# Kernel tuning notes

Hardware: AMD Instinct MI355X
Metric: run time of the kernel (lower is better)

The kernel has to match this reference:

```python
import jax, jax.numpy as jnp
import numpy as np

N_NODES = 50000
N_EDGES = 800000
NUM_GRAPHS = 250
NODES_PER_GRAPH = 200  # max_len for to_dense_batch
IN_DIM = 128
H1 = 128
H2 = 128
LSTM_H = 128
OUT_DIM = 2
NEG_SLOPE = 0.2  # PyG GATConv default leaky relu slope


def setup_inputs() -> dict:
    key = jax.random.key(0)
    ks = jax.random.split(key, 16)
    x = jax.random.normal(ks[0], (N_NODES, IN_DIM), dtype=jnp.float32)
    edge_index = jax.random.randint(ks[1], (2, N_EDGES), 0, N_NODES, dtype=jnp.int32)
    batch = (jnp.arange(N_NODES, dtype=jnp.int32) // NODES_PER_GRAPH)
    g = lambda k, shp, fan: jax.random.normal(k, shp, dtype=jnp.float32) / np.sqrt(fan)
    return {
        "x": x,
        "edge_index": edge_index,
        "batch": batch,
        "W_gat": g(ks[2], (IN_DIM, H1), IN_DIM),
        "a_src": g(ks[3], (H1,), H1),
        "a_dst": g(ks[4], (H1,), H1),
        "b_gat": jnp.zeros((H1,), jnp.float32),
        "W_gcn": g(ks[5], (H1, H2), H1),
        "b_gcn": jnp.zeros((H2,), jnp.float32),
        "W_ih": g(ks[6], (4 * LSTM_H, H2), H2),
        "W_hh": g(ks[7], (4 * LSTM_H, LSTM_H), LSTM_H),
        "b_ih": jnp.zeros((4 * LSTM_H,), jnp.float32),
        "b_hh": jnp.zeros((4 * LSTM_H,), jnp.float32),
        "W_fc": g(ks[8], (LSTM_H, OUT_DIM), LSTM_H),
        "b_fc": jnp.zeros((OUT_DIM,), jnp.float32),
    }


def _add_self_loops(edge_index, n):
    loop = jnp.arange(n, dtype=edge_index.dtype)
    src = jnp.concatenate([edge_index[0], loop])
    dst = jnp.concatenate([edge_index[1], loop])
    return src, dst


def _gat_conv(x, edge_index, W, a_src, a_dst, b):
    n = x.shape[0]
    h = x @ W                                  # [N, H1]
    src, dst = _add_self_loops(edge_index, n)
    alpha_s = h @ a_src                        # [N]
    alpha_d = h @ a_dst
    e = alpha_s[src] + alpha_d[dst]            # [E+N]
    e = jnp.where(e > 0, e, NEG_SLOPE * e)     # leaky relu
    # softmax over edges sharing the same destination node
    m = jax.ops.segment_max(e, dst, num_segments=n)
    ex = jnp.exp(e - m[dst])
    denom = jax.ops.segment_sum(ex, dst, num_segments=n)
    alpha = ex / denom[dst]
    out = jax.ops.segment_sum(h[src] * alpha[:, None], dst, num_segments=n)
    return out + b


def _gcn_conv(x, edge_index, W, b):
    n = x.shape[0]
    h = x @ W                                  # [N, H2]
    src, dst = _add_self_loops(edge_index, n)
    deg = jax.ops.segment_sum(jnp.ones_like(dst, dtype=h.dtype), dst, num_segments=n)
    dinv = jax.lax.rsqrt(jnp.maximum(deg, 1.0))
    coef = dinv[src] * dinv[dst]               # symmetric normalization
    out = jax.ops.segment_sum(h[src] * coef[:, None], dst, num_segments=n)
    return out + b


def _to_dense_batch(x, batch, num_graphs, max_len):
    n = x.shape[0]
    ones = jnp.ones((n,), jnp.int32)
    counts = jax.ops.segment_sum(ones, batch, num_segments=num_graphs)
    starts = jnp.cumsum(counts) - counts
    pos = jnp.arange(n, dtype=jnp.int32) - starts[batch]
    padded = jnp.zeros((num_graphs, max_len, x.shape[1]), x.dtype)
    padded = padded.at[batch, pos].set(x)
    return padded, counts


def _lstm_last_hidden(padded, lengths, W_ih, W_hh, b_ih, b_hh):
    B, T, D = padded.shape
    H = W_hh.shape[1]
    xs = jnp.swapaxes(padded, 0, 1)            # [T, B, D]

    def step(carry, x_t):
        h, c = carry
        gates = x_t @ W_ih.T + b_ih + h @ W_hh.T + b_hh
        i, f, g, o = jnp.split(gates, 4, axis=-1)
        c = jax.nn.sigmoid(f) * c + jax.nn.sigmoid(i) * jnp.tanh(g)
        h = jax.nn.sigmoid(o) * jnp.tanh(c)
        return (h, c), h

    init = (jnp.zeros((B, H), padded.dtype), jnp.zeros((B, H), padded.dtype))
    _, hs = jax.lax.scan(step, init, xs)       # hs: [T, B, H]
    # packed-sequence semantics: hidden state at each graph's last valid step
    return hs[lengths - 1, jnp.arange(B)]


def reference(x, edge_index, batch, W_gat, a_src, a_dst, b_gat, W_gcn, b_gcn,
              W_ih, W_hh, b_ih, b_hh, W_fc, b_fc):
    h = jax.nn.relu(_gat_conv(x, edge_index, W_gat, a_src, a_dst, b_gat))
    h = jax.nn.relu(_gcn_conv(h, edge_index, W_gcn, b_gcn))
    padded, lengths = _to_dense_batch(h, batch, NUM_GRAPHS, NODES_PER_GRAPH)
    g_rep = _lstm_last_hidden(padded, lengths, W_ih, W_hh, b_ih, b_hh)
    return g_rep @ W_fc + b_fc
```

## Files before the change

### kernel.cpp

```cpp
#include <hip/hip_runtime.h>
#include <cstddef>

#define NN 50000
#define NE 800000
#define NG 250
#define TT 200
#define DD 128
#define GH 512
#define NEG_SLOPE 0.2f
#define NCHUNK 4
#define CLEN 50
#define CAP 128
#define PSTRIDE 136

static __device__ __forceinline__ float fsig(float x) { return 1.0f / (1.0f + __expf(-x)); }
static __device__ __forceinline__ float ftanh(float x) {
    float e = __expf(2.0f * x);
    return 1.0f - 2.0f / (e + 1.0f);
}
static __device__ __forceinline__ unsigned short f2bf(float f) {
    unsigned int u = __float_as_uint(f);
    return (unsigned short)((u + 0x7fffu + ((u >> 16) & 1u)) >> 16);
}

static __device__ __forceinline__ void gll16(const float* src, float* ldsdst) {
    __builtin_amdgcn_global_load_lds(
        (const __attribute__((address_space(1))) void*)src,
        (__attribute__((address_space(3))) void*)ldsdst, 16, 0, 0);
}

__global__ void k_init(int* cnt, int* gstart, int n, int ng1) {
    int i = blockIdx.x * 256 + threadIdx.x;
    if (i < n) cnt[i] = 1;
    if (i < ng1) gstart[i] = n;
}

__global__ void k_transpose2(const float* __restrict__ inA, float* __restrict__ outA,
                             const float* __restrict__ inB, float* __restrict__ outB) {
    int b = blockIdx.x, k = threadIdx.x;
    if (b < DD) outA[b * DD + k] = inA[k * DD + b];
    else { int n = b - DD; outB[n * DD + k] = inB[k * DD + n]; }
}

__global__ __launch_bounds__(256) void k_gemm(
    const float* __restrict__ A, const float* __restrict__ B, float* __restrict__ C,
    int M, int N, int t0, int clen, int rowsPerGraph,
    const float* __restrict__ bias1, const float* __restrict__ bias2,
    unsigned short* __restrict__ Cbf,
    float* __restrict__ as_out, float* __restrict__ ad_out,
    const float* __restrict__ a_src, const float* __restrict__ a_dst)
{
    __shared__ float4 As[2][1024];
    __shared__ float4 Bs[2][1024];
    const int tid = threadIdx.x;
    const int wv = tid >> 6;
    const int m0 = blockIdx.x * 128, n0 = blockIdx.y * 128;
    const int tr = tid >> 4, tc = tid & 15;

    float acc[8][8];
    #pragma unroll
    for (int i = 0; i < 8; ++i)
        #pragma unroll
        for (int j = 0; j < 8; ++j) acc[i][j] = 0.f;

    auto stageA = [&](int buf, int k0) {
        #pragma unroll
        for (int it = 0; it < 4; ++it) {
            int f4 = it * 256 + tid;
            int r = f4 >> 3;
            int c4s = (f4 & 7) ^ (r & 7);
            int gr = m0 + r;
            float* dst = (float*)&As[buf][it * 256 + wv * 64];
            if (gr < M) {
                int flat = (gr / clen) * rowsPerGraph + t0 + (gr % clen);
                gll16(A + (size_t)flat * DD + k0 + c4s * 4, dst);
            }
        }
    };
    auto stageB = [&](int buf, int k0) {
        #pragma unroll
        for (int it = 0; it < 4; ++it) {
            int f4 = it * 256 + tid;
            int r = f4 >> 3;
            int c4s = (f4 & 7) ^ (r & 7);
            int gn = n0 + r;
            float* dst = (float*)&Bs[buf][it * 256 + wv * 64];
            if (gn < N) gll16(B + (size_t)gn * DD + k0 + c4s * 4, dst);
        }
    };

    stageA(0, 0); stageB(0, 0);
    __syncthreads();
    int buf = 0;
    const int axor = tr & 7;
    const int bxor = tc & 7;
    for (int ks = 0; ks < 4; ++ks) {
        if (ks < 3) { stageA(buf ^ 1, (ks + 1) * 32); stageB(buf ^ 1, (ks + 1) * 32); }
        const float4* Af = &As[buf][0];
        const float4* Bf = &Bs[buf][0];
        #pragma unroll 1
        for (int k4 = 0; k4 < 8; ++k4) {
            float4 a[8], b[8];
            #pragma unroll
            for (int i = 0; i < 8; ++i) a[i] = Af[(tr + i * 16) * 8 + (k4 ^ axor)];
            #pragma unroll
            for (int j = 0; j < 8; ++j) b[j] = Bf[(tc + j * 16) * 8 + (k4 ^ bxor)];
            #pragma unroll
            for (int i = 0; i < 8; ++i)
                #pragma unroll
                for (int j = 0; j < 8; ++j)
                    acc[i][j] += a[i].x * b[j].x + a[i].y * b[j].y + a[i].z * b[j].z + a[i].w * b[j].w;
        }
        __syncthreads();
        buf ^= 1;
    }

    if (as_out) {
        float asv[8], adv[8];
        #pragma unroll
        for (int j = 0; j < 8; ++j) { asv[j] = a_src[tc + 16 * j]; adv[j] = a_dst[tc + 16 * j]; }
        #pragma unroll
        for (int i = 0; i < 8; ++i) {
            float s = 0.f, d = 0.f;
            #pragma unroll
            for (int j = 0; j < 8; ++j) { s += acc[i][j] * asv[j]; d += acc[i][j] * adv[j]; }
            #pragma unroll
            for (int off = 1; off < 16; off <<= 1) { s += __shfl_xor(s, off); d += __shfl_xor(d, off); }
            int gr = m0 + tr + i * 16;
            if (tc == 0 && gr < M) { as_out[gr] = s; ad_out[gr] = d; }
        }
    }

    #pragma unroll
    for (int i = 0; i < 8; ++i) {
        int gr = m0 + tr + i * 16;
        if (gr >= M) continue;
        #pragma unroll
        for (int j = 0; j < 8; ++j) {
            int gn = n0 + tc + j * 16;
            if (gn >= N) continue;
            float v = acc[i][j];
            if (bias1) v += bias1[gn];
            if (bias2) v += bias2[gn];
            if (Cbf) Cbf[(size_t)gr * N + gn] = f2bf(v);
            else     C[(size_t)gr * N + gn] = v;
        }
    }
}

__global__ void k_hist(const int* __restrict__ ei, int* cnt, int E) {
    int e = blockIdx.x * 256 + threadIdx.x;
    if (e < E) atomicAdd(&cnt[ei[E + e]], 1);
}

__global__ __launch_bounds__(256) void k_scan1(const int* __restrict__ cnt, int* __restrict__ fill,
                                               int* __restrict__ bsum, int n) {
    __shared__ int wsum[4];
    int tid = threadIdx.x, lane = tid & 63, wv = tid >> 6;
    int i = blockIdx.x * 256 + tid;
    int v = (i < n) ? cnt[i] : 0;
    int sc = v;
    #pragma unroll
    for (int off = 1; off < 64; off <<= 1) {
        int t = __shfl_up(sc, off);
        if (lane >= off) sc += t;
    }
    if (lane == 63) wsum[wv] = sc;
    __syncthreads();
    int base = 0;
    if (wv > 0) base += wsum[0];
    if (wv > 1) base += wsum[1];
    if (wv > 2) base += wsum[2];
    if (i < n) fill[i] = base + sc - v;
    if (tid == 255) bsum[blockIdx.x] = base + sc;
}
__global__ __launch_bounds__(256) void k_scan2(int* __restrict__ bsum, int nb) {
    __shared__ int wsum[4];
    int tid = threadIdx.x, lane = tid & 63, wv = tid >> 6;
    int v = (tid < nb) ? bsum[tid] : 0;
    int sc = v;
    #pragma unroll
    for (int off = 1; off < 64; off <<= 1) {
        int t = __shfl_up(sc, off);
        if (lane >= off) sc += t;
    }
    if (lane == 63) wsum[wv] = sc;
    __syncthreads();
    int base = 0;
    if (wv > 0) base += wsum[0];
    if (wv > 1) base += wsum[1];
    if (wv > 2) base += wsum[2];
    if (tid < nb) bsum[tid] = base + sc - v;
}
__global__ void k_scan3(const int* __restrict__ bsum, const int* __restrict__ cnt,
                        int* __restrict__ rp, int* __restrict__ fill,
                        float* __restrict__ dinv, const int* __restrict__ batch,
                        int* __restrict__ gstart, int n) {
    int i = blockIdx.x * 256 + threadIdx.x;
    if (i >= n) return;
    int v = fill[i] + bsum[blockIdx.x];
    rp[i] = v;
    fill[i] = v;
    if (i == n - 1) rp[n] = v + cnt[i];
    dinv[i] = rsqrtf(fmaxf((float)cnt[i], 1.0f));
    int b = batch[i];
    if (i == 0 || batch[i - 1] != b) gstart[b] = i;
}

__global__ void k_fill(const int* __restrict__ ei, int* fill, int* esrc, int E, int N) {
    int i = blockIdx.x * 256 + threadIdx.x;
    if (i < E) {
        int s = ei[i], d = ei[E + i];
        int slot = atomicAdd(&fill[d], 1);
        esrc[slot] = s;
    } else if (i < E + N) {
        int v = i - E;
        int slot = atomicAdd(&fill[v], 1);
        esrc[slot] = v;
    }
}

__global__ __launch_bounds__(256) void k_gat(
    const unsigned int* __restrict__ h1b,
    const float* __restrict__ as, const float* __restrict__ ad_,
    const int* __restrict__ rp, const int* __restrict__ esrc,
    const float* __restrict__ bias, float* __restrict__ out, int n)
{
    __shared__ float2 ws_sh[4][CAP];
    int wv = threadIdx.x >> 6;
    int node = blockIdx.x * 4 + wv;
    int lane = threadIdx.x & 63;
    if (node >= n) return;
    int r0 = rp[node], r1 = rp[node + 1];
    int deg = r1 - r0;
    float adv = ad_[node];

    float sum = 0.f;
    for (int base = 0; base < deg; base += 64) {
        int idx = base + lane;
        float ex = 0.f;
        if (idx < deg) {
            int s = esrc[r0 + idx];
            float e = as[s] + adv;
            e = e > 0.f ? e : NEG_SLOPE * e;
            ex = __expf(e);
            if (idx < CAP) ws_sh[wv][idx] = make_float2(ex, __int_as_float(s));
        }
        sum += ex;
    }
    #pragma unroll
    for (int off = 1; off < 64; off <<= 1) sum += __shfl_xor(sum, off);
    float inv = 1.0f / sum;

    int nser = deg < CAP ? deg : CAP;
    int npad = (nser + 7) & ~7;
    for (int p = nser + lane; p < npad; p += 64)
        ws_sh[wv][p] = make_float2(0.f, __int_as_float(0));

    float ax = 0.f, ay = 0.f;
    float wa[8]; unsigned int va[8];
    #pragma unroll
    for (int u = 0; u < 8; ++u) {
        float2 t = ws_sh[wv][u];
        wa[u] = t.x; va[u] = h1b[(size_t)__float_as_int(t.y) * 64 + lane];
    }
    #pragma unroll 1
    for (int idx = 8; idx < npad; idx += 8) {
        float wb[8]; unsigned int vb[8];
        #pragma unroll
        for (int u = 0; u < 8; ++u) {
            float2 t = ws_sh[wv][idx + u];
            wb[u] = t.x; vb[u] = h1b[(size_t)__float_as_int(t.y) * 64 + lane];
        }
        #pragma unroll
        for (int u = 0; u < 8; ++u) {
            ax += wa[u] * __uint_as_float(va[u] << 16);
            ay += wa[u] * __uint_as_float(va[u] & 0xffff0000u);
        }
        #pragma unroll
        for (int u = 0; u < 8; ++u) { wa[u] = wb[u]; va[u] = vb[u]; }
    }
    #pragma unroll
    for (int u = 0; u < 8; ++u) {
        ax += wa[u] * __uint_as_float(va[u] << 16);
        ay += wa[u] * __uint_as_float(va[u] & 0xffff0000u);
    }

    for (int j = r0 + CAP; j < r1; ++j) {
        int s = esrc[j];
        float e = as[s] + adv;
        e = e > 0.f ? e : NEG_SLOPE * e;
        float w = __expf(e);
        unsigned int v = h1b[(size_t)s * 64 + lane];
        ax += w * __uint_as_float(v << 16);
        ay += w * __uint_as_float(v & 0xffff0000u);
    }
    float2 bv = *(const float2*)(bias + 2 * lane);
    float2 o;
    o.x = fmaxf(ax * inv + bv.x, 0.f);
    o.y = fmaxf(ay * inv + bv.y, 0.f);
    *(float2*)(out + (size_t)node * DD + 2 * lane) = o;
}

__global__ __launch_bounds__(256) void k_gcn(
    const unsigned int* __restrict__ h2b, const float* __restrict__ dinv,
    const int* __restrict__ rp, const int* __restrict__ esrc,
    const float* __restrict__ bias, const int* __restrict__ batch,
    const int* __restrict__ gstart, float* __restrict__ padded, int n)
{
    __shared__ float2 cs_sh[4][CAP];
    int wv = threadIdx.x >> 6;
    int node = blockIdx.x * 4 + wv;
    int lane = threadIdx.x & 63;
    if (node >= n) return;
    int r0 = rp[node], r1 = rp[node + 1];
    int deg = r1 - r0;
    float dn = dinv[node];

    for (int base = 0; base < deg; base += 64) {
        int idx = base + lane;
        if (idx < deg && idx < CAP) {
            int s = esrc[r0 + idx];
            cs_sh[wv][idx] = make_float2(dinv[s], __int_as_float(s));
        }
    }
    int nser = deg < CAP ? deg : CAP;
    int npad = (nser + 7) & ~7;
    for (int p = nser + lane; p < npad; p += 64)
        cs_sh[wv][p] = make_float2(0.f, __int_as_float(0));
    __syncthreads();

    float ax = 0.f, ay = 0.f;
    float wa[8]; unsigned int va[8];
    #pragma unroll
    for (int u = 0; u < 8; ++u) {
        float2 t = cs_sh[wv][u];
        wa[u] = t.x; va[u] = h2b[(size_t)__float_as_int(t.y) * 64 + lane];
    }
    #pragma unroll 1
    for (int idx = 8; idx < npad; idx += 8) {
        float wb[8]; unsigned int vb[8];
        #pragma unroll
        for (int u = 0; u < 8; ++u) {
            float2 t = cs_sh[wv][idx + u];
            wb[u] = t.x; vb[u] = h2b[(size_t)__float_as_int(t.y) * 64 + lane];
        }
        #pragma unroll
        for (int u = 0; u < 8; ++u) {
            ax += wa[u] * __uint_as_float(va[u] << 16);
            ay += wa[u] * __uint_as_float(va[u] & 0xffff0000u);
        }
        #pragma unroll
        for (int u = 0; u < 8; ++u) { wa[u] = wb[u]; va[u] = vb[u]; }
    }
    #pragma unroll
    for (int u = 0; u < 8; ++u) {
        ax += wa[u] * __uint_as_float(va[u] << 16);
        ay += wa[u] * __uint_as_float(va[u] & 0xffff0000u);
    }

    for (int j = r0 + CAP; j < r1; ++j) {
        int s = esrc[j];
        float c = dinv[s];
        unsigned int v = h2b[(size_t)s * 64 + lane];
        ax += c * __uint_as_float(v << 16);
        ay += c * __uint_as_float(v & 0xffff0000u);
    }
    int g = batch[node];
    if (g < 0 || g >= NG) return;
    int p = node - gstart[g];
    if (p < 0 || p >= TT) return;
    float2 bv = *(const float2*)(bias + 2 * lane);
    float2 o;
    o.x = fmaxf(ax * dn + bv.x, 0.f);
    o.y = fmaxf(ay * dn + bv.y, 0.f);
    *(float2*)(padded + ((size_t)g * TT + p) * DD + 2 * lane) = o;
}

__global__ __launch_bounds__(512) void k_lstm(
    const float* __restrict__ xw,
    const float* __restrict__ Whh,
    const int* __restrict__ gstart,
    float* __restrict__ hstate, float* __restrict__ cstate,
    float* __restrict__ grep, int t0, int clen)
{
    int g = blockIdx.x, tid = threadIdx.x;
    __shared__ __align__(16) float h_sh[DD];
    __shared__ __align__(16) float part[4][4 * PSTRIDE];

    const int seg = tid >> 7;
    const int gq  = tid & 127;
    const int qt  = gq >> 5;
    const int ub  = (gq & 31) * 4;
    const int u   = tid >> 2;
    const int q   = tid & 3;
    const int lane = tid & 63;
    const int qbase = lane & ~3;

    float4 w[4][8];
    #pragma unroll
    for (int g4 = 0; g4 < 4; ++g4)
        #pragma unroll
        for (int i = 0; i < 8; ++i)
            w[g4][i] = *(const float4*)(Whh + (size_t)(4 * gq + g4) * DD + seg * 32 + i * 4);

    float creg = 0.f, hn = 0.f;
    if (t0 == 0) {
        if (tid < DD) h_sh[tid] = 0.f;
    } else {
        creg = cstate[g * DD + u];
        hn = hstate[g * DD + u];
        if (q == 0) h_sh[u] = hn;
    }
    int take = gstart[g + 1] - gstart[g] - 1;
    if (take < 0) take = 0;
    if (take > TT - 1) take = TT - 1;
    __syncthreads();

    const float* xb = xw + (size_t)g * clen * GH + q * DD + u;
    float xv = xb[0];

    for (int t = t0; t < t0 + clen; ++t) {
        int rel = t - t0;
        float xvn = 0.f;
        if (rel + 1 < clen) xvn = xb[(size_t)(rel + 1) * GH];

        float4 hseg[8];
        #pragma unroll
        for (int i = 0; i < 8; ++i) hseg[i] = *(const float4*)(h_sh + seg * 32 + i * 4);
        float p0 = 0.f, p1 = 0.f, p2 = 0.f, p3 = 0.f;
        #pragma unroll
        for (int i = 0; i < 8; ++i) {
            float4 h4 = hseg[i];
            p0 += h4.x * w[0][i].x + h4.y * w[0][i].y + h4.z * w[0][i].z + h4.w * w[0][i].w;
            p1 += h4.x * w[1][i].x + h4.y * w[1][i].y + h4.z * w[1][i].z + h4.w * w[1][i].w;
            p2 += h4.x * w[2][i].x + h4.y * w[2][i].y + h4.z * w[2][i].z + h4.w * w[2][i].w;
            p3 += h4.x * w[3][i].x + h4.y * w[3][i].y + h4.z * w[3][i].z + h4.w * w[3][i].w;
        }
        *(float4*)(&part[seg][qt * PSTRIDE + ub]) = make_float4(p0, p1, p2, p3);
        __syncthreads();

        int pidx = q * PSTRIDE + u;
        float G = xv + part[0][pidx] + part[1][pidx] + part[2][pidx] + part[3][pidx];
        float a = (q == 2) ? 2.f : -1.f;
        float e = __expf(a * G);
        float act = (q == 2) ? (1.f - 2.f / (e + 1.f)) : (1.f / (1.f + e));
        float ai = __shfl(act, qbase + 0);
        float af = __shfl(act, qbase + 1);
        float ag = __shfl(act, qbase + 2);
        float ao = __shfl(act, qbase + 3);
        creg = af * creg + ai * ag;
        hn = ao * ftanh(creg);
        if (q == 0) {
            h_sh[u] = hn;
            if (t == take) grep[g * DD + u] = hn;
        }
        xv = xvn;
        __syncthreads();
    }
    if (q == 0) { hstate[g * DD + u] = hn; cstate[g * DD + u] = creg; }
}

__global__ void k_fc(const float* __restrict__ grep, const float* __restrict__ Wfc,
                     const float* __restrict__ bfc, float* __restrict__ out, int G) {
    int i = blockIdx.x * 256 + threadIdx.x;
    if (i >= G * 2) return;
    int g = i >> 1, o = i & 1;
    float acc = bfc[o];
    for (int d = 0; d < DD; ++d) acc += grep[g * DD + d] * Wfc[d * 2 + o];
    out[i] = acc;
}

extern "C" void kernel_launch(void* const* d_in, const int* in_sizes, int n_in,
                              void* d_out, int out_size, void* d_ws, size_t ws_size,
                              hipStream_t stream) {
    const float* x     = (const float*)d_in[0];
    const int*   ei    = (const int*)d_in[1];
    const int*   batch = (const int*)d_in[2];
    const float* Wgat  = (const float*)d_in[3];
    const float* a_src = (const float*)d_in[4];
    const float* a_dst = (const float*)d_in[5];
    const float* b_gat = (const float*)d_in[6];
    const float* Wgcn  = (const float*)d_in[7];
    const float* b_gcn = (const float*)d_in[8];
    const float* Wih   = (const float*)d_in[9];
    const float* Whh   = (const float*)d_in[10];
    const float* b_ih  = (const float*)d_in[11];
    const float* b_hh  = (const float*)d_in[12];
    const float* Wfc   = (const float*)d_in[13];
    const float* b_fc  = (const float*)d_in[14];
    float* out = (float*)d_out;

    float* ws = (float*)d_ws;
    const size_t F = (size_t)NN * DD;
    unsigned short* h1b = (unsigned short*)ws;
    unsigned short* h2b = (unsigned short*)ws;
    float* xwChunk = ws;
    float* gato   = ws + F;
    float* padded = ws + F;
    size_t off = 2 * F;
    float* alpha_s = ws + off; off += 50048;
    float* alpha_d = ws + off; off += 50048;
    float* dinv    = ws + off; off += 50048;
    int*   cnt     = (int*)(ws + off); off += 50048;
    int*   rp      = (int*)(ws + off); off += 50056;
    int*   fill    = (int*)(ws + off); off += 50048;
    int*   esrc    = (int*)(ws + off); off += 850048;
    int*   bsum    = (int*)(ws + off); off += 256;
    int*   gstart  = (int*)(ws + off); off += 256;
    float* grep    = ws + off; off += 32000;
    float* hstate  = ws + off; off += 32000;
    float* cstate  = ws + off; off += 32000;
    float* WgatT   = ws + off; off += 16384;
    float* WgcnT   = ws + off; off += 16384;
    const size_t xwBigFloats = (size_t)NG * TT * GH;
    float* xwBig = ws + off;
    const bool big = ws_size >= (off + xwBigFloats) * sizeof(float);

    k_transpose2<<<256, 128, 0, stream>>>(Wgat, WgatT, Wgcn, WgcnT);

    k_gemm<<<dim3(391, 1), 256, 0, stream>>>(x, WgatT, nullptr, NN, DD, 0, TT, TT,
                                             nullptr, nullptr, h1b,
                                             alpha_s, alpha_d, a_src, a_dst);

    k_init<<<196, 256, 0, stream>>>(cnt, gstart, NN, NG + 1);
    k_hist<<<3125, 256, 0, stream>>>(ei, cnt, NE);
    k_scan1<<<196, 256, 0, stream>>>(cnt, fill, bsum, NN);
    k_scan2<<<1, 256, 0, stream>>>(bsum, 196);
    k_scan3<<<196, 256, 0, stream>>>(bsum, cnt, rp, fill, dinv, batch, gstart, NN);
    k_fill<<<3321, 256, 0, stream>>>(ei, fill, esrc, NE, NN);

    k_gat<<<12500, 256, 0, stream>>>((const unsigned int*)h1b, alpha_s, alpha_d,
                                     rp, esrc, b_gat, gato, NN);

    k_gemm<<<dim3(391, 1), 256, 0, stream>>>(gato, WgcnT, nullptr, NN, DD, 0, TT, TT,
                                             nullptr, nullptr, h2b,
                                             nullptr, nullptr, nullptr, nullptr);

    k_gcn<<<12500, 256, 0, stream>>>((const unsigned int*)h2b, dinv, rp, esrc,
                                     b_gcn, batch, gstart, padded, NN);

    if (big) {
        k_gemm<<<dim3(391, 4), 256, 0, stream>>>(padded, Wih, xwBig, NG * TT, GH,
                                                 0, TT, TT, b_ih, b_hh,
                                                 nullptr, nullptr, nullptr, nullptr, nullptr);
        k_lstm<<<NG, 512, 0, stream>>>(xwBig, Whh, gstart, hstate, cstate, grep, 0, TT);
    } else {
        for (int c = 0; c < NCHUNK; ++c) {
            int t0 = c * CLEN;
            k_gemm<<<dim3(98, 4), 256, 0, stream>>>(padded, Wih, xwChunk, NG * CLEN, GH,
                                                    t0, CLEN, TT, b_ih, b_hh,
                                                    nullptr, nullptr, nullptr, nullptr, nullptr);
            k_lstm<<<NG, 512, 0, stream>>>(xwChunk, Whh, gstart, hstate, cstate, grep, t0, CLEN);
        }
    }

    k_fc<<<2, 256, 0, stream>>>(grep, Wfc, b_fc, out, NG);
}
```

Measured before the change: 577.2 us.

## Batch 16 graphs per block in LSTM recurrence using split-bf16 MFMA

Adds a new LSTM kernel that processes 16 graphs per block and computes the recurrent h@W_hh product with bf16 MFMA instructions. It keeps fp32-like accuracy by splitting weights and hidden state into hi/lo bf16 parts and issuing three MFMAs per tile. W_hh stays in registers, the hidden state is double-buffered in swizzled LDS, and the next step's input projection is prefetched. The goal is to cut the serial per-step cost of the recurrence, which was done with scalar FMAs, one graph per block. In exchange only 16 blocks are launched, so the GPU is heavily underused, and the split-bf16 scheme carries a small precision risk.

```diff
diff --git a/kernel.cpp b/kernel.cpp
--- a/kernel.cpp
+++ b/kernel.cpp
@@ -12,6 +12,10 @@
 #define CLEN 50
 #define CAP 128
 #define PSTRIDE 136
+#define GB 16
+
+typedef __attribute__((ext_vector_type(8))) short bf16x8;
+typedef __attribute__((ext_vector_type(4))) float f32x4;
 
 static __device__ __forceinline__ float fsig(float x) { return 1.0f / (1.0f + __expf(-x)); }
 static __device__ __forceinline__ float ftanh(float x) {
@@ -21,6 +25,9 @@
 static __device__ __forceinline__ unsigned short f2bf(float f) {
     unsigned int u = __float_as_uint(f);
     return (unsigned short)((u + 0x7fffu + ((u >> 16) & 1u)) >> 16);
+}
+static __device__ __forceinline__ float bf2f(unsigned short b) {
+    return __uint_as_float(((unsigned int)b) << 16);
 }
 
 static __device__ __forceinline__ void gll16(const float* src, float* ldsdst) {
@@ -377,9 +384,121 @@
     *(float2*)(padded + ((size_t)g * TT + p) * DD + 2 * lane) = o;
 }
 
-__global__ __launch_bounds__(512) void k_lstm(
+__global__ __launch_bounds__(512, 1) void k_lstm_mfma(
     const float* __restrict__ xw,
     const float* __restrict__ Whh,
+    const int* __restrict__ gstart,
+    float* __restrict__ grep)
+{
+    const int tid = threadIdx.x;
+    const int w = tid >> 6;
+    const int l = tid & 63;
+    const int col = l & 15;
+    const int kg = l >> 4;
+    const int g = blockIdx.x * GB + col;
+    const int gc = g < NG ? g : NG - 1;
+    const int urow = kg * 4;
+
+    __shared__ unsigned short hh[2][16 * 128];
+    __shared__ unsigned short hl[2][16 * 128];
+
+    bf16x8 whi[4][4], wlo[4][4];
+    #pragma unroll
+    for (int q = 0; q < 4; ++q) {
+        const float* wrow = Whh + (size_t)(q * DD + 16 * w + col) * DD;
+        #pragma unroll
+        for (int ks = 0; ks < 4; ++ks) {
+            float4 f0 = *(const float4*)(wrow + ks * 32 + kg * 8);
+            float4 f1 = *(const float4*)(wrow + ks * 32 + kg * 8 + 4);
+            float ff[8] = {f0.x, f0.y, f0.z, f0.w, f1.x, f1.y, f1.z, f1.w};
+            #pragma unroll
+            for (int j = 0; j < 8; ++j) {
+                unsigned short hi = f2bf(ff[j]);
+                whi[q][ks][j] = (short)hi;
+                wlo[q][ks][j] = (short)f2bf(ff[j] - bf2f(hi));
+            }
+        }
+    }
+
+    for (int i = tid; i < 16 * 128; i += 512) { hh[0][i] = 0; hl[0][i] = 0; }
+
+    int take = gstart[gc + 1] - gstart[gc] - 1;
+    if (take < 0) take = 0;
+    if (take > TT - 1) take = TT - 1;
+
+    float c0 = 0.f, c1 = 0.f, c2 = 0.f, c3 = 0.f;
+
+    const float* xbase = xw + (size_t)gc * TT * GH + 16 * w + urow;
+    float4 xq[4];
+    #pragma unroll
+    for (int q = 0; q < 4; ++q) xq[q] = *(const float4*)(xbase + q * DD);
+
+    const int swz = (col & 7) << 4;
+    __syncthreads();
+
+    int cur = 0;
+    for (int t = 0; t < TT; ++t) {
+        float4 xn[4];
+        if (t + 1 < TT) {
+            const float* xr = xbase + (size_t)(t + 1) * GH;
+            #pragma unroll
+            for (int q = 0; q < 4; ++q) xn[q] = *(const float4*)(xr + q * DD);
+        }
+        bf16x8 bhi[4], blo[4];
+        #pragma unroll
+        for (int ks = 0; ks < 4; ++ks) {
+            int idx = col * 128 + (((ks * 64 + kg * 16) ^ swz) >> 1);
+            bhi[ks] = *(const bf16x8*)(&hh[cur][idx]);
+            blo[ks] = *(const bf16x8*)(&hl[cur][idx]);
+        }
+        f32x4 acc[4];
+        #pragma unroll
+        for (int q = 0; q < 4; ++q) {
+            acc[q][0] = xq[q].x; acc[q][1] = xq[q].y; acc[q][2] = xq[q].z; acc[q][3] = xq[q].w;
+        }
+        #pragma unroll
+        for (int q = 0; q < 4; ++q)
+            #pragma unroll
+            for (int ks = 0; ks < 4; ++ks) {
+                acc[q] = __builtin_amdgcn_mfma_f32_16x16x32_bf16(whi[q][ks], bhi[ks], acc[q], 0, 0, 0);
+                acc[q] = __builtin_amdgcn_mfma_f32_16x16x32_bf16(whi[q][ks], blo[ks], acc[q], 0, 0, 0);
+                acc[q] = __builtin_amdgcn_mfma_f32_16x16x32_bf16(wlo[q][ks], bhi[ks], acc[q], 0, 0, 0);
+            }
+        float hv[4];
+        {
+            float ci[4] = {c0, c1, c2, c3};
+            #pragma unroll
+            for (int r = 0; r < 4; ++r) {
+                float cc = fsig(acc[1][r]) * ci[r] + fsig(acc[0][r]) * ftanh(acc[2][r]);
+                hv[r] = fsig(acc[3][r]) * ftanh(cc);
+                ci[r] = cc;
+            }
+            c0 = ci[0]; c1 = ci[1]; c2 = ci[2]; c3 = ci[3];
+        }
+        {
+            int idx = col * 128 + (((2 * (16 * w + urow)) ^ swz) >> 1);
+            unsigned short vh[4], vl[4];
+            #pragma unroll
+            for (int r = 0; r < 4; ++r) {
+                vh[r] = f2bf(hv[r]);
+                vl[r] = f2bf(hv[r] - bf2f(vh[r]));
+            }
+            *(ushort4*)(&hh[cur ^ 1][idx]) = make_ushort4(vh[0], vh[1], vh[2], vh[3]);
+            *(ushort4*)(&hl[cur ^ 1][idx]) = make_ushort4(vl[0], vl[1], vl[2], vl[3]);
+        }
+        if (t == take && g < NG) {
+            *(float4*)(grep + (size_t)g * DD + 16 * w + urow) =
+                make_float4(hv[0], hv[1], hv[2], hv[3]);
+        }
+        #pragma unroll
+        for (int q = 0; q < 4; ++q) xq[q] = xn[q];
+        cur ^= 1;
+        __syncthreads();
+    }
+}
+
+__global__ __launch_bounds__(512) void k_lstm(
+    const float* __restrict__ xw, const float* __restrict__ Whh,
     const int* __restrict__ gstart,
     float* __restrict__ hstate, float* __restrict__ cstate,
     float* __restrict__ grep, int t0, int clen)
@@ -544,7 +663,7 @@
         k_gemm<<<dim3(391, 4), 256, 0, stream>>>(padded, Wih, xwBig, NG * TT, GH,
                                                  0, TT, TT, b_ih, b_hh,
                                                  nullptr, nullptr, nullptr, nullptr, nullptr);
-        k_lstm<<<NG, 512, 0, stream>>>(xwBig, Whh, gstart, hstate, cstate, grep, 0, TT);
+        k_lstm_mfma<<<(NG + GB - 1) / GB, 512, 0, stream>>>(xwBig, Whh, gstart, grep);
     } else {
         for (int c = 0; c < NCHUNK; ++c) {
             int t0 = c * CLEN;
```

Result: slower. 825.3 us (+43.0%).

## Use split-bf16 MFMA GEMM for LSTM input projection

Applied to the files above, without the earlier changes.

Replaces the FP32 scalar GEMM computing the LSTM input projection (padded @ W_ih^T + biases) with a matrix-core kernel using bf16 MFMA 16x16x32. Near-FP32 accuracy is kept by a three-term split (A_hi*B_hi + A_lo*B_hi + A_hi*B_lo), with the A tile staged in swizzled LDS through global_load_lds. This targets the cost of a 50000x512x128 FP32 GEMM on vector ALUs, at the price of three MFMA passes plus per-element bf16 conversion work. It only applies on the 'big' path; the chunked path still uses the old GEMM.

```diff
diff --git a/kernel.cpp b/kernel.cpp
--- a/kernel.cpp
+++ b/kernel.cpp
@@ -13,6 +13,9 @@
 #define CAP 128
 #define PSTRIDE 136
 
+typedef __attribute__((ext_vector_type(8))) short bf16x8;
+typedef __attribute__((ext_vector_type(4))) float f32x4;
+
 static __device__ __forceinline__ float fsig(float x) { return 1.0f / (1.0f + __expf(-x)); }
 static __device__ __forceinline__ float ftanh(float x) {
     float e = __expf(2.0f * x);
@@ -21,6 +24,9 @@
 static __device__ __forceinline__ unsigned short f2bf(float f) {
     unsigned int u = __float_as_uint(f);
     return (unsigned short)((u + 0x7fffu + ((u >> 16) & 1u)) >> 16);
+}
+static __device__ __forceinline__ float bf2f(unsigned short b) {
+    return __uint_as_float(((unsigned int)b) << 16);
 }
 
 static __device__ __forceinline__ void gll16(const float* src, float* ldsdst) {
@@ -148,6 +154,124 @@
     }
 }
 
+__global__ __launch_bounds__(256) void k_gemm_mx(
+    const float* __restrict__ A, const float* __restrict__ Bw, float* __restrict__ C,
+    int M, int N, const float* __restrict__ bias1, const float* __restrict__ bias2)
+{
+    __shared__ float4 As[4096];
+    const int tid = threadIdx.x;
+    const int wv = tid >> 6;
+    const int l = tid & 63;
+    const int m0 = blockIdx.x * 128, n0 = blockIdx.y * 128;
+    const int wr = (wv >> 1) * 64, wc = (wv & 1) * 64;
+    const int lr = l & 15, kg = l >> 4;
+
+    #pragma unroll
+    for (int it = 0; it < 16; ++it) {
+        int f4 = it * 256 + tid;
+        int r = f4 >> 5, c4 = f4 & 31;
+        int c4s = c4 ^ (r & 7);
+        int gr = m0 + r;
+        float* dst = (float*)&As[it * 256 + wv * 64];
+        if (gr < M) gll16(A + (size_t)gr * DD + c4s * 4, dst);
+    }
+
+    bf16x8 bh[4][4];
+    #pragma unroll
+    for (int ct = 0; ct < 4; ++ct) {
+        const float* brow = Bw + (size_t)(n0 + wc + ct * 16 + lr) * DD;
+        #pragma unroll
+        for (int ks = 0; ks < 4; ++ks) {
+            float4 f0 = *(const float4*)(brow + ks * 32 + kg * 8);
+            float4 f1 = *(const float4*)(brow + ks * 32 + kg * 8 + 4);
+            float ff[8] = {f0.x, f0.y, f0.z, f0.w, f1.x, f1.y, f1.z, f1.w};
+            #pragma unroll
+            for (int j = 0; j < 8; ++j) bh[ct][ks][j] = (short)f2bf(ff[j]);
+        }
+    }
+    __syncthreads();
+
+    f32x4 acc[4][4];
+    #pragma unroll
+    for (int rt = 0; rt < 4; ++rt)
+        #pragma unroll
+        for (int ct = 0; ct < 4; ++ct) acc[rt][ct] = (f32x4){0.f, 0.f, 0.f, 0.f};
+
+    #pragma unroll 1
+    for (int ks = 0; ks < 4; ++ks) {
+        bf16x8 ahi[4], alo[4];
+        #pragma unroll
+        for (int rt = 0; rt < 4; ++rt) {
+            int row = wr + rt * 16 + lr;
+            int qb = ks * 8 + kg * 2;
+            float4 f0 = As[row * 32 + (qb ^ (row & 7))];
+            float4 f1 = As[row * 32 + ((qb + 1) ^ (row & 7))];
+            float ff[8] = {f0.x, f0.y, f0.z, f0.w, f1.x, f1.y, f1.z, f1.w};
+            #pragma unroll
+            for (int j = 0; j < 8; ++j) {
+                unsigned short hi = f2bf(ff[j]);
+                ahi[rt][j] = (short)hi;
+                alo[rt][j] = (short)f2bf(ff[j] - bf2f(hi));
+            }
+        }
+        #pragma unroll
+        for (int rt = 0; rt < 4; ++rt)
+            #pragma unroll
+            for (int ct = 0; ct < 4; ++ct) {
+                acc[rt][ct] = __builtin_amdgcn_mfma_f32_16x16x32_bf16(ahi[rt], bh[ct][ks], acc[rt][ct], 0, 0, 0);
+                acc[rt][ct] = __builtin_amdgcn_mfma_f32_16x16x32_bf16(alo[rt], bh[ct][ks], acc[rt][ct], 0, 0, 0);
+            }
+    }
+
+    #pragma unroll
+    for (int ct = 0; ct < 4; ++ct) {
+        const float* brow = Bw + (size_t)(n0 + wc + ct * 16 + lr) * DD;
+        #pragma unroll
+        for (int ks = 0; ks < 4; ++ks) {
+            float4 f0 = *(const float4*)(brow + ks * 32 + kg * 8);
+            float4 f1 = *(const float4*)(brow + ks * 32 + kg * 8 + 4);
+            float ff[8] = {f0.x, f0.y, f0.z, f0.w, f1.x, f1.y, f1.z, f1.w};
+            #pragma unroll
+            for (int j = 0; j < 8; ++j)
+                bh[ct][ks][j] = (short)f2bf(ff[j] - bf2f(f2bf(ff[j])));
+        }
+    }
+
+    #pragma unroll 1
+    for (int ks = 0; ks < 4; ++ks) {
+        bf16x8 ahi[4];
+        #pragma unroll
+        for (int rt = 0; rt < 4; ++rt) {
+            int row = wr + rt * 16 + lr;
+            int qb = ks * 8 + kg * 2;
+            float4 f0 = As[row * 32 + (qb ^ (row & 7))];
+            float4 f1 = As[row * 32 + ((qb + 1) ^ (row & 7))];
+            float ff[8] = {f0.x, f0.y, f0.z, f0.w, f1.x, f1.y, f1.z, f1.w};
+            #pragma unroll
+            for (int j = 0; j < 8; ++j) ahi[rt][j] = (short)f2bf(ff[j]);
+        }
+        #pragma unroll
+        for (int rt = 0; rt < 4; ++rt)
+            #pragma unroll
+            for (int ct = 0; ct < 4; ++ct)
+                acc[rt][ct] = __builtin_amdgcn_mfma_f32_16x16x32_bf16(ahi[rt], bh[ct][ks], acc[rt][ct], 0, 0, 0);
+    }
+
+    #pragma unroll
+    for (int ct = 0; ct < 4; ++ct) {
+        int col = n0 + wc + ct * 16 + lr;
+        float bsum = bias1[col] + bias2[col];
+        #pragma unroll
+        for (int rt = 0; rt < 4; ++rt) {
+            #pragma unroll
+            for (int r = 0; r < 4; ++r) {
+                int row = m0 + wr + rt * 16 + kg * 4 + r;
+                if (row < M) C[(size_t)row * N + col] = acc[rt][ct][r] + bsum;
+            }
+        }
+    }
+}
+
 __global__ void k_hist(const int* __restrict__ ei, int* cnt, int E) {
     int e = blockIdx.x * 256 + threadIdx.x;
     if (e < E) atomicAdd(&cnt[ei[E + e]], 1);
@@ -378,8 +502,7 @@
 }
 
 __global__ __launch_bounds__(512) void k_lstm(
-    const float* __restrict__ xw,
-    const float* __restrict__ Whh,
+    const float* __restrict__ xw, const float* __restrict__ Whh,
     const int* __restrict__ gstart,
     float* __restrict__ hstate, float* __restrict__ cstate,
     float* __restrict__ grep, int t0, int clen)
@@ -541,9 +664,8 @@
                                      b_gcn, batch, gstart, padded, NN);
 
     if (big) {
-        k_gemm<<<dim3(391, 4), 256, 0, stream>>>(padded, Wih, xwBig, NG * TT, GH,
-                                                 0, TT, TT, b_ih, b_hh,
-                                                 nullptr, nullptr, nullptr, nullptr, nullptr);
+        k_gemm_mx<<<dim3(391, 4), 256, 0, stream>>>(padded, Wih, xwBig, NG * TT, GH,
+                                                    b_ih, b_hh);
         k_lstm<<<NG, 512, 0, stream>>>(xwBig, Whh, gstart, hstate, cstate, grep, 0, TT);
     } else {
         for (int c = 0; c < NCHUNK; ++c) {
```

New measurement: 550.7 us. 1.05x faster.
